# Optimization experiments

Hardware: AMD Instinct MI355X
Metric: run time of the kernel (lower is better)

## Reference

```python
import jax, jax.numpy as jnp
import numpy as np
from math import sqrt

B, TS_D, SEG, D, H = 16, 2, 1024, 256, 8
D_FF = 1024
DK = D // H
EPS = 1e-5


def _layernorm(x, g, b):
    mu = jnp.mean(x, axis=-1, keepdims=True)
    var = jnp.mean(jnp.square(x - mu), axis=-1, keepdims=True)
    return (x - mu) * jax.lax.rsqrt(var + EPS) * g + b


def setup_inputs() -> dict:
    key = jax.random.key(0)
    ks = jax.random.split(key, 16)
    s = 0.02
    return {
        "x": jax.random.normal(ks[0], (B, TS_D, SEG, D), dtype=jnp.float32),
        "Wq": jax.random.normal(ks[1], (D, D), dtype=jnp.float32) * s,
        "bq": jnp.zeros((D,), jnp.float32),
        "Wk": jax.random.normal(ks[2], (D, D), dtype=jnp.float32) * s,
        "bk": jnp.zeros((D,), jnp.float32),
        "Wv": jax.random.normal(ks[3], (D, D), dtype=jnp.float32) * s,
        "bv": jnp.zeros((D,), jnp.float32),
        "Wo": jax.random.normal(ks[4], (D, D), dtype=jnp.float32) * s,
        "bo": jnp.zeros((D,), jnp.float32),
        "g31": jnp.ones((D,), jnp.float32),
        "b31": jnp.zeros((D,), jnp.float32),
        "W1": jax.random.normal(ks[5], (D, D_FF), dtype=jnp.float32) * s,
        "b1": jnp.zeros((D_FF,), jnp.float32),
        "W2": jax.random.normal(ks[6], (D_FF, D), dtype=jnp.float32) * s,
        "b2": jnp.zeros((D,), jnp.float32),
        "g41": jnp.ones((D,), jnp.float32),
        "b41": jnp.zeros((D,), jnp.float32),
    }


def reference(x, Wq, bq, Wk, bk, Wv, bv, Wo, bo, g31, b31, W1, b1, W2, b2, g41, b41):
    # x: [B, ts_d=2, seg, d]; output is final_out2 (only live path of the module)
    b, ts_d, seg, d = x.shape
    scale = 1.0 / sqrt(DK)
    segments = x.reshape(b, ts_d * seg, d)            # [B, 2*seg, d]
    Q = (segments @ Wq + bq).reshape(b, -1, H, DK)
    K = (segments @ Wk + bk).reshape(b, -1, H, DK)
    V = (segments @ Wv + bv).reshape(b, -1, H, DK)
    q = Q[:, :seg]       # first seg positions (channel 0)
    k = K[:, -seg:]      # last seg positions (channel 1)
    v = V[:, -seg:]
    # cross-segment dual attention
    A1 = jax.nn.softmax(scale * jnp.einsum('blhe,bshe->bhls', q, k), axis=-1)
    out1 = jnp.einsum('bhls,bshd->blhd', A1, v).reshape(b, seg, d)
    A2 = jax.nn.softmax(scale * jnp.einsum('blhe,bshe->bhls', k, q), axis=-1)
    out2 = jnp.einsum('bhls,bshd->blhd', A2, q).reshape(b, seg, d)
    y = jnp.concatenate([out1, out2], axis=1) @ Wo + bo   # [B, 2*seg, d]
    h = _layernorm(segments + y, g31, b31)
    mlp = jax.nn.gelu(h @ W1 + b1, approximate=False) @ W2 + b2
    h = _layernorm(h + mlp, g41, b41)
    return h.reshape(b, ts_d, seg, d)
```

## Files before the change

### kernel.cpp

```cpp
#include <hip/hip_runtime.h>
#include <hip/hip_bf16.h>
#include <math.h>

#define BATCH 16
#define SEG 1024
#define DMODEL 256
#define NH 8
#define DK 32
#define DFF 1024
#define NTOK (BATCH * 2 * SEG)
#define EPS 1e-5f

typedef __attribute__((ext_vector_type(8))) short short8;
typedef __attribute__((ext_vector_type(4))) short short4b;
typedef __attribute__((ext_vector_type(4))) float f32x4;

#if __has_builtin(__builtin_amdgcn_exp2f)
#define EXP2(x) __builtin_amdgcn_exp2f(x)
#else
#define EXP2(x) __expf((x) * 0.6931471805599453f)
#endif

__device__ __forceinline__ ushort f2bf(float x) {
    union { float f; unsigned u; } a; a.f = x;
    unsigned r = a.u + 0x7fffu + ((a.u >> 16) & 1u);
    return (ushort)(r >> 16);
}

typedef const __attribute__((address_space(1))) unsigned gas_u32;
typedef __attribute__((address_space(3))) unsigned las_u32;
__device__ __forceinline__ void gload_lds16(const ushort* g, ushort* l) {
    __builtin_amdgcn_global_load_lds((gas_u32*)g, (las_u32*)l, 16, 0, 0);
}

__global__ __launch_bounds__(256) void wfrag_all_kernel(
    const float* __restrict__ Wq, const float* __restrict__ Wk,
    const float* __restrict__ Wv, const float* __restrict__ Wo,
    const float* __restrict__ W1, const float* __restrict__ W2,
    ushort* __restrict__ Wqf, ushort* __restrict__ Wkf,
    ushort* __restrict__ Wvf, ushort* __restrict__ Wof,
    ushort* __restrict__ W1f, ushort* __restrict__ W2f)
{
    const int blk = blockIdx.x;
    const float* src; ushort* dst; int K, N, order, base;
    if (blk < 32)       { src = Wq; dst = Wqf; K = 256;  N = 256;  order = 0; base = 0;   }
    else if (blk < 64)  { src = Wk; dst = Wkf; K = 256;  N = 256;  order = 0; base = 32;  }
    else if (blk < 96)  { src = Wv; dst = Wvf; K = 256;  N = 256;  order = 0; base = 64;  }
    else if (blk < 128) { src = Wo; dst = Wof; K = 256;  N = 256;  order = 0; base = 96;  }
    else if (blk < 256) { src = W1; dst = W1f; K = 256;  N = 1024; order = 0; base = 128; }
    else                { src = W2; dst = W2f; K = 1024; N = 256;  order = 1; base = 256; }
    const int tid = (blk - base) * 256 + threadIdx.x;
    const int KT_ = K >> 5, NT_ = N >> 4;
    const int lane = tid & 63;
    const int frag = tid >> 6;
    int kt, nt;
    if (order) { kt = frag / NT_; nt = frag % NT_; }
    else       { nt = frag / KT_; kt = frag % KT_; }
    const int quad = lane >> 4, l = lane & 15;
    const float* s = src + (size_t)(kt * 32 + quad * 8) * N + nt * 16 + l;
    short8 v;
#pragma unroll
    for (int j = 0; j < 8; j++) v[j] = (short)f2bf(s[(size_t)j * N]);
    *(short8*)&dst[(size_t)tid * 8] = v;
}

#define ASTR 264

__device__ __forceinline__ void dense256_pass(
    const ushort* __restrict__ Wf, ushort* WL, const short8* af,
    f32x4* acc, int t, int w, int lane)
{
#pragma unroll
    for (int nt = 0; nt < 16; ++nt) acc[nt] = (f32x4){0.f, 0.f, 0.f, 0.f};
    {
        const ushort* g = Wf + (size_t)w * 4096 + lane * 8;
        ushort* ld = WL + w * 4096;
#pragma unroll
        for (int i = 0; i < 8; ++i) gload_lds16(g + i * 512, ld + i * 512);
    }
    __syncthreads();
    for (int c = 0; c < 4; ++c) {
        if (c < 3) {
            const ushort* g = Wf + (size_t)(c + 1) * 16384 + w * 4096 + lane * 8;
            ushort* ld = WL + ((c + 1) & 1) * 8192 + w * 4096;
#pragma unroll
            for (int i = 0; i < 8; ++i) gload_lds16(g + i * 512, ld + i * 512);
        }
        const ushort* buf = WL + (c & 1) * 8192;
#pragma unroll
        for (int n2 = 0; n2 < 4; ++n2)
#pragma unroll
            for (int kt = 0; kt < 8; ++kt) {
                const short8 bf_ = *(const short8*)&buf[(n2 * 8 + kt) * 512 + lane * 8];
                acc[c * 4 + n2] = __builtin_amdgcn_mfma_f32_16x16x32_bf16(af[kt], bf_, acc[c * 4 + n2], 0, 0, 0);
            }
        __syncthreads();
    }
}

__global__ __launch_bounds__(256) void qkv_mfma_kernel(
    const float* __restrict__ x,
    const ushort* __restrict__ Wqf, const float* __restrict__ bq,
    const ushort* __restrict__ Wkf, const float* __restrict__ bk,
    const ushort* __restrict__ Wvf, const float* __restrict__ bv,
    ushort* __restrict__ qbuf, ushort* __restrict__ kbuf,
    ushort* __restrict__ qt, ushort* __restrict__ vt)
{
    __shared__ __align__(16) ushort SM[64 * ASTR];
    const int bid = blockIdx.x;
    const int which = bid >> 8;
    const int sub = bid & 255;
    const int b = sub >> 4, ti = sub & 15;
    const int half = (which == 0) ? 0 : 1;
    const int t = threadIdx.x;
    const int w = t >> 6, lane = t & 63, l = lane & 15, quad = lane >> 4;

    const float* xrow = x + ((size_t)b * 2048 + (size_t)half * 1024 + ti * 64) * 256;
#pragma unroll
    for (int p = 0; p < 16; ++p) {
        int ch = t + 256 * p;
        int row = ch >> 6, c4 = ch & 63;
        float4 v = *(const float4*)&xrow[row * 256 + c4 * 4];
        uint2 pk;
        pk.x = (unsigned)f2bf(v.x) | ((unsigned)f2bf(v.y) << 16);
        pk.y = (unsigned)f2bf(v.z) | ((unsigned)f2bf(v.w) << 16);
        *(uint2*)&SM[row * ASTR + c4 * 4] = pk;
    }
    __syncthreads();

    short8 af[8];
#pragma unroll
    for (int kt = 0; kt < 8; ++kt)
        af[kt] = *(const short8*)&SM[(w * 16 + l) * ASTR + kt * 32 + quad * 8];
    __syncthreads();

    const ushort* Wf  = (which == 0) ? Wqf : (which == 1 ? Wkf : Wvf);
    const float* bias = (which == 0) ? bq  : (which == 1 ? bk  : bv);
    const float kscale = (which == 1) ? 0.25503472f : 1.0f;

    f32x4 acc[16];
    dense256_pass(Wf, SM, af, acc, t, w, lane);

    ushort bfv[16][4];
#pragma unroll
    for (int nt = 0; nt < 16; ++nt) {
        const float bb = bias[nt * 16 + l];
#pragma unroll
        for (int r = 0; r < 4; ++r) bfv[nt][r] = f2bf((acc[nt][r] + bb) * kscale);
    }

    if (which <= 1) {
        ushort* obuf = which ? kbuf : qbuf;
#pragma unroll
        for (int nt = 0; nt < 16; ++nt) {
            const int h = nt >> 1, e = (nt & 1) * 16 + l;
#pragma unroll
            for (int r = 0; r < 4; ++r) {
                int tok = ti * 64 + w * 16 + quad * 4 + r;
                obuf[(((size_t)b * 8 + h) * SEG + tok) * 32 + e] = bfv[nt][r];
            }
        }
    }
    if (which != 1) {
        ushort* tb = which ? vt : qt;
#pragma unroll
        for (int nt = 0; nt < 16; ++nt)
#pragma unroll
            for (int r = 0; r < 4; ++r)
                SM[(nt * 16 + l) * 66 + w * 16 + quad * 4 + r] = bfv[nt][r];
        __syncthreads();
        const int d = t, hh = t >> 5, e = t & 31;
        ushort* dr = tb + (((size_t)b * 8 + hh) * 32 + e) * 1024 + ti * 64;
#pragma unroll
        for (int j = 0; j < 8; ++j) {
            uint2 v;
            v.x = *(const unsigned*)&SM[d * 66 + j * 8];
            v.y = *(const unsigned*)&SM[d * 66 + j * 8 + 2];
            unsigned z0 = *(const unsigned*)&SM[d * 66 + j * 8 + 4];
            unsigned z1 = *(const unsigned*)&SM[d * 66 + j * 8 + 6];
            *(uint4*)&dr[j * 8] = make_uint4(v.x, v.y, z0, z1);
        }
    }
}

#define KTILE 128
#define KP 40
#define VP 132

__global__ __launch_bounds__(256) void attn_mfma_kernel(
    const ushort* __restrict__ qbuf, const ushort* __restrict__ kbuf,
    const ushort* __restrict__ qt, const ushort* __restrict__ vt,
    ushort* __restrict__ abuf)
{
    __shared__ __align__(16) ushort Kl[KTILE * KP];
    __shared__ __align__(16) ushort Vl[32 * VP];

    const int bid   = blockIdx.x;
    const int sbh   = bid & 255;
    const int qtile = bid >> 8;
    const int stage = sbh >> 7;
    const int b     = (sbh >> 3) & 15;
    const int h     = sbh & 7;

    const ushort* Qm = stage ? kbuf : qbuf;
    const ushort* Km = stage ? qbuf : kbuf;
    const ushort* Vt = stage ? qt : vt;
    const size_t bh = ((size_t)b * 8 + h) * SEG * 32;

    const int t    = threadIdx.x;
    const int w    = t >> 6;
    const int lane = t & 63;
    const int l    = lane & 15;
    const int quad = lane >> 4;

    const int qrow = qtile * 64 + w * 16 + l;
    const short8 qf = *(const short8*)&Qm[bh + (size_t)qrow * 32 + quad * 8];

    f32x4 o0 = {0.f, 0.f, 0.f, 0.f};
    f32x4 o1 = {0.f, 0.f, 0.f, 0.f};
    f32x4 o2 = {0.f, 0.f, 0.f, 0.f};
    const short4b ones = {(short)0x3F80, (short)0x3F80, (short)0x3F80, (short)0x3F80};

    const int ch0 = t, ch1 = t + 256;
    const int kr0 = ((ch0 >> 6) << 4) | (ch0 & 15), kp0 = (ch0 >> 4) & 3;
    const int kr1 = ((ch1 >> 6) << 4) | (ch1 & 15), kp1 = (ch1 >> 4) & 3;
    const int vd0 = ch0 >> 4, vc0 = ch0 & 15;
    const int vd1 = ch1 >> 4, vc1 = ch1 & 15;
    const ushort* Kgb = &Km[bh];
    const ushort* Vgb = &Vt[bh];

    short8 rk0 = *(const short8*)&Kgb[(size_t)kr0 * 32 + kp0 * 8];
    short8 rk1 = *(const short8*)&Kgb[(size_t)kr1 * 32 + kp1 * 8];
    short8 rv0 = *(const short8*)&Vgb[(size_t)vd0 * 1024 + vc0 * 8];
    short8 rv1 = *(const short8*)&Vgb[(size_t)vd1 * 1024 + vc1 * 8];

    for (int tile = 0; tile < 8; ++tile) {
        __syncthreads();
        *(short8*)&Kl[kr0 * KP + kp0 * 8] = rk0;
        *(short8*)&Kl[kr1 * KP + kp1 * 8] = rk1;
        *(short8*)&Vl[vd0 * VP + vc0 * 8] = rv0;
        *(short8*)&Vl[vd1 * VP + vc1 * 8] = rv1;
        __syncthreads();

        if (tile < 7) {
            const size_t ko = (size_t)(tile + 1) * KTILE * 32;
            const size_t vo = (size_t)(tile + 1) * KTILE;
            rk0 = *(const short8*)&Kgb[ko + (size_t)kr0 * 32 + kp0 * 8];
            rk1 = *(const short8*)&Kgb[ko + (size_t)kr1 * 32 + kp1 * 8];
            rv0 = *(const short8*)&Vgb[vo + (size_t)vd0 * 1024 + vc0 * 8];
            rv1 = *(const short8*)&Vgb[vo + (size_t)vd1 * 1024 + vc1 * 8];
        }

#pragma unroll
        for (int kb = 0; kb < 8; ++kb) {
            const short8 kf = *(const short8*)&Kl[(kb * 16 + l) * KP + quad * 8];
            f32x4 z = {0.f, 0.f, 0.f, 0.f};
            f32x4 sc = __builtin_amdgcn_mfma_f32_16x16x32_bf16(kf, qf, z, 0, 0, 0);
            union { float f; unsigned u; } a0, a1, a2, a3;
            a0.f = EXP2(sc[0]); a1.f = EXP2(sc[1]);
            a2.f = EXP2(sc[2]); a3.f = EXP2(sc[3]);
            unsigned lo = __builtin_amdgcn_perm(a1.u, a0.u, 0x07060302u);
            unsigned hi = __builtin_amdgcn_perm(a3.u, a2.u, 0x07060302u);
            union { uint2 u; short4b s; } pk; pk.u = make_uint2(lo, hi);
            const short4b vf0 = *(const short4b*)&Vl[l * VP + kb * 16 + quad * 4];
            const short4b vf1 = *(const short4b*)&Vl[(16 + l) * VP + kb * 16 + quad * 4];
            o0 = __builtin_amdgcn_mfma_f32_16x16x16bf16_1k(vf0, pk.s, o0, 0, 0, 0);
            o1 = __builtin_amdgcn_mfma_f32_16x16x16bf16_1k(vf1, pk.s, o1, 0, 0, 0);
            o2 = __builtin_amdgcn_mfma_f32_16x16x16bf16_1k(ones, pk.s, o2, 0, 0, 0);
        }
    }

    const float inv = 1.0f / o2[0];
#pragma unroll
    for (int r = 0; r < 4; ++r) { o0[r] *= inv; o1[r] *= inv; }

    __syncthreads();
    ushort* Ob = &Kl[w * 16 * 40];
#pragma unroll
    for (int r = 0; r < 4; ++r) {
        Ob[l * 40 + quad * 4 + r]      = f2bf(o0[r]);
        Ob[l * 40 + 16 + quad * 4 + r] = f2bf(o1[r]);
    }
    __syncthreads();
    const int q = lane >> 2, part = lane & 3;
    const short8 ov = *(const short8*)&Ob[q * 40 + part * 8];
    const int tok = qtile * 64 + w * 16 + q;
    *(short8*)&abuf[((size_t)b * 2 * SEG + (size_t)stage * SEG + tok) * 256 + h * 32 + part * 8] = ov;
}

#define GP 40

__global__ __launch_bounds__(256, 2) void proj_mlp_kernel(
    const ushort* __restrict__ abuf, const ushort* __restrict__ Wof,
    const float* __restrict__ bo, const float* __restrict__ x,
    const float* __restrict__ g31, const float* __restrict__ b31,
    const ushort* __restrict__ W1f, const float* __restrict__ b1,
    const ushort* __restrict__ W2f, const float* __restrict__ b2,
    const float* __restrict__ g41, const float* __restrict__ b41,
    float* __restrict__ io)
{
    __shared__ __align__(16) ushort SM[2 * 16384];
    __shared__ __align__(16) ushort G[4][16 * GP];
    __shared__ __align__(16) float B1L[DFF];
    const int bid = blockIdx.x;
    const size_t tok0 = (size_t)bid * 64;
    const int t = threadIdx.x;
    const int w = t >> 6, lane = t & 63, l = lane & 15, quad = lane >> 4;

#pragma unroll
    for (int p = 0; p < 8; ++p) {
        int ch = t + 256 * p;
        int row = ch >> 5, c8 = ch & 31;
        *(short8*)&SM[row * ASTR + c8 * 8] = *(const short8*)&abuf[(tok0 + row) * 256 + c8 * 8];
    }
    *(float4*)&B1L[t * 4] = *(const float4*)&b1[t * 4];
    __syncthreads();

    short8 af[8];
#pragma unroll
    for (int kt = 0; kt < 8; ++kt)
        af[kt] = *(const short8*)&SM[(w * 16 + l) * ASTR + kt * 32 + quad * 8];
    __syncthreads();

    f32x4 acc[16];
    dense256_pass(Wof, SM, af, acc, t, w, lane);

#pragma unroll
    for (int nt = 0; nt < 16; ++nt) {
        const int d = nt * 16 + l;
        const float bv = bo[d];
#pragma unroll
        for (int r = 0; r < 4; ++r) {
            size_t tok = tok0 + w * 16 + quad * 4 + r;
            acc[nt][r] += bv + x[tok * 256 + d];
        }
    }
    {
        float mu_[4], is_[4];
#pragma unroll
        for (int r = 0; r < 4; ++r) {
            float s = 0.f;
#pragma unroll
            for (int nt = 0; nt < 16; ++nt) s += acc[nt][r];
            s += __shfl_xor(s, 1); s += __shfl_xor(s, 2);
            s += __shfl_xor(s, 4); s += __shfl_xor(s, 8);
            float mu = s * (1.0f / 256.0f);
            float vs = 0.f;
#pragma unroll
            for (int nt = 0; nt < 16; ++nt) { float dd = acc[nt][r] - mu; vs += dd * dd; }
            vs += __shfl_xor(vs, 1); vs += __shfl_xor(vs, 2);
            vs += __shfl_xor(vs, 4); vs += __shfl_xor(vs, 8);
            mu_[r] = mu;
            is_[r] = rsqrtf(vs * (1.0f / 256.0f) + EPS);
        }
#pragma unroll
        for (int nt = 0; nt < 16; ++nt) {
            const int d = nt * 16 + l;
            const float gg = g31[d], bb = b31[d];
#pragma unroll
            for (int r = 0; r < 4; ++r) {
                float hv = (acc[nt][r] - mu_[r]) * is_[r] * gg + bb;
                acc[nt][r] = hv;
                SM[(w * 16 + quad * 4 + r) * ASTR + d] = f2bf(hv);
            }
        }
    }
    __syncthreads();
#pragma unroll
    for (int kt = 0; kt < 8; ++kt)
        af[kt] = *(const short8*)&SM[(w * 16 + l) * ASTR + kt * 32 + quad * 8];
    __syncthreads();

    f32x4 out[16];
#pragma unroll
    for (int nt = 0; nt < 16; ++nt) out[nt] = (f32x4){0.f, 0.f, 0.f, 0.f};

    ushort* Gw = &G[w][0];

    {
        const ushort* g1 = W1f + w * 2048 + lane * 8;
        const ushort* g2 = W2f + w * 2048 + lane * 8;
        ushort* l1 = SM + w * 2048;
        ushort* l2 = SM + 8192 + w * 2048;
#pragma unroll
        for (int i = 0; i < 4; ++i) {
            gload_lds16(g1 + i * 512, l1 + i * 512);
            gload_lds16(g2 + i * 512, l2 + i * 512);
        }
    }
    __syncthreads();

    for (int c = 0; c < 32; ++c) {
        if (c < 31) {
            const int nb = (c + 1) & 1;
            const ushort* g1 = W1f + (size_t)(c + 1) * 8192 + w * 2048 + lane * 8;
            ushort* l1 = SM + nb * 16384 + w * 2048;
            const ushort* g2 = W2f + (size_t)(c + 1) * 8192 + w * 2048 + lane * 8;
            ushort* l2 = SM + nb * 16384 + 8192 + w * 2048;
#pragma unroll
            for (int i = 0; i < 4; ++i) {
                gload_lds16(g1 + i * 512, l1 + i * 512);
                gload_lds16(g2 + i * 512, l2 + i * 512);
            }
        }
        const ushort* WL = SM + (c & 1) * 16384;

        f32x4 s0 = {0.f, 0.f, 0.f, 0.f};
        f32x4 s1 = {0.f, 0.f, 0.f, 0.f};
#pragma unroll
        for (int kt = 0; kt < 8; ++kt) {
            const short8 b0 = *(const short8*)&WL[kt * 512 + lane * 8];
            const short8 b1_ = *(const short8*)&WL[(8 + kt) * 512 + lane * 8];
            s0 = __builtin_amdgcn_mfma_f32_16x16x32_bf16(af[kt], b0, s0, 0, 0, 0);
            s1 = __builtin_amdgcn_mfma_f32_16x16x32_bf16(af[kt], b1_, s1, 0, 0, 0);
        }

#pragma unroll
        for (int n2 = 0; n2 < 2; ++n2) {
            const float bv = B1L[c * 32 + n2 * 16 + l];
#pragma unroll
            for (int r = 0; r < 4; ++r) {
                float v = (n2 ? s1[r] : s0[r]) + bv;
                float au = fabsf(v) * 0.70710678118654752f;
                float t1 = __builtin_amdgcn_rcpf(fmaf(0.3275911f, au, 1.0f));
                float e  = EXP2(au * au * -1.4426950408889634f);
                float p5 = fmaf(fmaf(fmaf(fmaf(1.061405429f, t1, -1.453152027f),
                                t1, 1.421413741f), t1, -0.284496736f), t1, 0.254829592f) * t1;
                float erf_abs = fmaf(-p5, e, 1.0f);
                float gl = fmaf(0.5f * fabsf(v), erf_abs, 0.5f * v);
                Gw[(quad * 4 + r) * GP + n2 * 16 + l] = f2bf(gl);
            }
        }

        const short8 gf = *(const short8*)&Gw[l * GP + quad * 8];
#pragma unroll
        for (int nt = 0; nt < 16; ++nt) {
            const short8 bf_ = *(const short8*)&WL[8192 + nt * 512 + lane * 8];
            out[nt] = __builtin_amdgcn_mfma_f32_16x16x32_bf16(gf, bf_, out[nt], 0, 0, 0);
        }
        __syncthreads();
    }

#pragma unroll
    for (int nt = 0; nt < 16; ++nt) {
        const int d = nt * 16 + l;
        const float bv = b2[d];
#pragma unroll
        for (int r = 0; r < 4; ++r)
            out[nt][r] += bv + acc[nt][r];
    }

    float mu_[4], is_[4];
#pragma unroll
    for (int r = 0; r < 4; ++r) {
        float s = 0.f;
#pragma unroll
        for (int nt = 0; nt < 16; ++nt) s += out[nt][r];
        s += __shfl_xor(s, 1); s += __shfl_xor(s, 2);
        s += __shfl_xor(s, 4); s += __shfl_xor(s, 8);
        float mu = s * (1.0f / 256.0f);
        float vs = 0.f;
#pragma unroll
        for (int nt = 0; nt < 16; ++nt) { float dd = out[nt][r] - mu; vs += dd * dd; }
        vs += __shfl_xor(vs, 1); vs += __shfl_xor(vs, 2);
        vs += __shfl_xor(vs, 4); vs += __shfl_xor(vs, 8);
        mu_[r] = mu;
        is_[r] = rsqrtf(vs * (1.0f / 256.0f) + EPS);
    }

#pragma unroll
    for (int nt = 0; nt < 16; ++nt) {
        const int d = nt * 16 + l;
        const float gg = g41[d], bb = b41[d];
#pragma unroll
        for (int r = 0; r < 4; ++r) {
            size_t tok = tok0 + w * 16 + quad * 4 + r;
            io[tok * 256 + d] = (out[nt][r] - mu_[r]) * is_[r] * gg + bb;
        }
    }
}

extern "C" void kernel_launch(void* const* d_in, const int* in_sizes, int n_in,
                              void* d_out, int out_size, void* d_ws, size_t ws_size,
                              hipStream_t stream)
{
    const float* x   = (const float*)d_in[0];
    const float* Wq  = (const float*)d_in[1];
    const float* bq  = (const float*)d_in[2];
    const float* Wk  = (const float*)d_in[3];
    const float* bk  = (const float*)d_in[4];
    const float* Wv  = (const float*)d_in[5];
    const float* bv  = (const float*)d_in[6];
    const float* Wo  = (const float*)d_in[7];
    const float* bo  = (const float*)d_in[8];
    const float* g31 = (const float*)d_in[9];
    const float* b31 = (const float*)d_in[10];
    const float* W1  = (const float*)d_in[11];
    const float* b1  = (const float*)d_in[12];
    const float* W2  = (const float*)d_in[13];
    const float* b2  = (const float*)d_in[14];
    const float* g41 = (const float*)d_in[15];
    const float* b41 = (const float*)d_in[16];

    float* out = (float*)d_out;

    const size_t HALF = (size_t)BATCH * SEG * DMODEL;
    ushort* qbuf = (ushort*)d_ws;
    ushort* kbuf = qbuf + HALF;
    ushort* qt   = kbuf + HALF;
    ushort* vt   = qt + HALF;
    ushort* abuf = vt + HALF;
    ushort* Wqf  = abuf + 2 * HALF;
    ushort* Wkf  = Wqf + 65536;
    ushort* Wvf  = Wkf + 65536;
    ushort* Wof  = Wvf + 65536;
    ushort* W1f  = Wof + 65536;
    ushort* W2f  = W1f + 262144;

    wfrag_all_kernel<<<384, 256, 0, stream>>>(Wq, Wk, Wv, Wo, W1, W2,
                                              Wqf, Wkf, Wvf, Wof, W1f, W2f);

    qkv_mfma_kernel<<<768, 256, 0, stream>>>(x, Wqf, bq, Wkf, bk, Wvf, bv,
                                             qbuf, kbuf, qt, vt);
    attn_mfma_kernel<<<2 * BATCH * NH * (SEG / 64), 256, 0, stream>>>(qbuf, kbuf, qt, vt, abuf);
    proj_mlp_kernel<<<NTOK / 64, 256, 0, stream>>>(abuf, Wof, bo, x, g31, b31,
                                                   W1f, b1, W2f, b2, g41, b41, out);
}
```

Measured before the change: 266.1 us.

## Double block tokens to 128 with 512 threads and triple-buffer MLP weight pipeline

Each proj_mlp block now handles 128 tokens with 8 waves, so every weight tile staged into LDS is reused by twice as many rows and global weight traffic is halved. The Wo projection is rewritten as an inline double-buffered LDS-staged loop. The W1/W2 chunk loop moves from double to triple buffering, with explicit vmcnt waits and raw barriers so loads run two chunks ahead. LDS use grows to about 96KB+ per block, which may cut occupancy, and the hand-coded waitcnt logic is fragile.

```diff
diff --git a/kernel.cpp b/kernel.cpp
--- a/kernel.cpp
+++ b/kernel.cpp
@@ -290,7 +290,7 @@
 
 #define GP 40
 
-__global__ __launch_bounds__(256, 2) void proj_mlp_kernel(
+__global__ __launch_bounds__(512, 2) void proj_mlp_kernel(
     const ushort* __restrict__ abuf, const ushort* __restrict__ Wof,
     const float* __restrict__ bo, const float* __restrict__ x,
     const float* __restrict__ g31, const float* __restrict__ b31,
@@ -299,21 +299,21 @@
     const float* __restrict__ g41, const float* __restrict__ b41,
     float* __restrict__ io)
 {
-    __shared__ __align__(16) ushort SM[2 * 16384];
-    __shared__ __align__(16) ushort G[4][16 * GP];
+    __shared__ __align__(16) ushort SM[3 * 16384];
+    __shared__ __align__(16) ushort G[8][16 * GP];
     __shared__ __align__(16) float B1L[DFF];
     const int bid = blockIdx.x;
-    const size_t tok0 = (size_t)bid * 64;
+    const size_t tok0 = (size_t)bid * 128;
     const int t = threadIdx.x;
     const int w = t >> 6, lane = t & 63, l = lane & 15, quad = lane >> 4;
 
 #pragma unroll
     for (int p = 0; p < 8; ++p) {
-        int ch = t + 256 * p;
+        int ch = t + 512 * p;
         int row = ch >> 5, c8 = ch & 31;
         *(short8*)&SM[row * ASTR + c8 * 8] = *(const short8*)&abuf[(tok0 + row) * 256 + c8 * 8];
     }
-    *(float4*)&B1L[t * 4] = *(const float4*)&b1[t * 4];
+    *(float2*)&B1L[t * 2] = *(const float2*)&b1[t * 2];
     __syncthreads();
 
     short8 af[8];
@@ -323,7 +323,32 @@
     __syncthreads();
 
     f32x4 acc[16];
-    dense256_pass(Wof, SM, af, acc, t, w, lane);
+#pragma unroll
+    for (int nt = 0; nt < 16; ++nt) acc[nt] = (f32x4){0.f, 0.f, 0.f, 0.f};
+    {
+        const ushort* g = Wof + (size_t)w * 2048 + lane * 8;
+        ushort* ld = SM + w * 2048;
+#pragma unroll
+        for (int i = 0; i < 4; ++i) gload_lds16(g + i * 512, ld + i * 512);
+    }
+    __syncthreads();
+    for (int c = 0; c < 4; ++c) {
+        if (c < 3) {
+            const ushort* g = Wof + (size_t)(c + 1) * 16384 + w * 2048 + lane * 8;
+            ushort* ld = SM + ((c + 1) & 1) * 16384 + w * 2048;
+#pragma unroll
+            for (int i = 0; i < 4; ++i) gload_lds16(g + i * 512, ld + i * 512);
+        }
+        const ushort* buf = SM + (c & 1) * 16384;
+#pragma unroll
+        for (int n2 = 0; n2 < 4; ++n2)
+#pragma unroll
+            for (int kt = 0; kt < 8; ++kt) {
+                const short8 bf_ = *(const short8*)&buf[(n2 * 8 + kt) * 512 + lane * 8];
+                acc[c * 4 + n2] = __builtin_amdgcn_mfma_f32_16x16x32_bf16(af[kt], bf_, acc[c * 4 + n2], 0, 0, 0);
+            }
+        __syncthreads();
+    }
 
 #pragma unroll
     for (int nt = 0; nt < 16; ++nt) {
@@ -377,33 +402,36 @@
 
     ushort* Gw = &G[w][0];
 
+    const int wo = w * 1024 + lane * 8;
+    const int wl = w * 1024;
+
     {
-        const ushort* g1 = W1f + w * 2048 + lane * 8;
-        const ushort* g2 = W2f + w * 2048 + lane * 8;
-        ushort* l1 = SM + w * 2048;
-        ushort* l2 = SM + 8192 + w * 2048;
-#pragma unroll
-        for (int i = 0; i < 4; ++i) {
-            gload_lds16(g1 + i * 512, l1 + i * 512);
-            gload_lds16(g2 + i * 512, l2 + i * 512);
-        }
-    }
-    __syncthreads();
+        const ushort* g1 = W1f + wo;            ushort* l1 = SM + wl;
+        const ushort* g2 = W2f + wo;            ushort* l2 = SM + 8192 + wl;
+        gload_lds16(g1, l1); gload_lds16(g1 + 512, l1 + 512);
+        gload_lds16(g2, l2); gload_lds16(g2 + 512, l2 + 512);
+    }
+    {
+        const ushort* g1 = W1f + 8192 + wo;     ushort* l1 = SM + 16384 + wl;
+        const ushort* g2 = W2f + 8192 + wo;     ushort* l2 = SM + 16384 + 8192 + wl;
+        gload_lds16(g1, l1); gload_lds16(g1 + 512, l1 + 512);
+        gload_lds16(g2, l2); gload_lds16(g2 + 512, l2 + 512);
+    }
+    asm volatile("s_waitcnt vmcnt(4)" ::: "memory");
+    __builtin_amdgcn_s_barrier();
+    __builtin_amdgcn_sched_barrier(0);
 
     for (int c = 0; c < 32; ++c) {
-        if (c < 31) {
-            const int nb = (c + 1) & 1;
-            const ushort* g1 = W1f + (size_t)(c + 1) * 8192 + w * 2048 + lane * 8;
-            ushort* l1 = SM + nb * 16384 + w * 2048;
-            const ushort* g2 = W2f + (size_t)(c + 1) * 8192 + w * 2048 + lane * 8;
-            ushort* l2 = SM + nb * 16384 + 8192 + w * 2048;
-#pragma unroll
-            for (int i = 0; i < 4; ++i) {
-                gload_lds16(g1 + i * 512, l1 + i * 512);
-                gload_lds16(g2 + i * 512, l2 + i * 512);
-            }
-        }
-        const ushort* WL = SM + (c & 1) * 16384;
+        if (c < 30) {
+            const int s = (c + 2) % 3;
+            const ushort* g1 = W1f + (size_t)(c + 2) * 8192 + wo;
+            ushort* l1 = SM + s * 16384 + wl;
+            const ushort* g2 = W2f + (size_t)(c + 2) * 8192 + wo;
+            ushort* l2 = SM + s * 16384 + 8192 + wl;
+            gload_lds16(g1, l1); gload_lds16(g1 + 512, l1 + 512);
+            gload_lds16(g2, l2); gload_lds16(g2 + 512, l2 + 512);
+        }
+        const ushort* WL = SM + (c % 3) * 16384;
 
         f32x4 s0 = {0.f, 0.f, 0.f, 0.f};
         f32x4 s1 = {0.f, 0.f, 0.f, 0.f};
@@ -438,7 +466,11 @@
             const short8 bf_ = *(const short8*)&WL[8192 + nt * 512 + lane * 8];
             out[nt] = __builtin_amdgcn_mfma_f32_16x16x32_bf16(gf, bf_, out[nt], 0, 0, 0);
         }
-        __syncthreads();
+
+        if (c < 30) { asm volatile("s_waitcnt vmcnt(4)" ::: "memory"); }
+        else        { asm volatile("s_waitcnt vmcnt(0)" ::: "memory"); }
+        __builtin_amdgcn_s_barrier();
+        __builtin_amdgcn_sched_barrier(0);
     }
 
 #pragma unroll
@@ -523,6 +555,6 @@
     qkv_mfma_kernel<<<768, 256, 0, stream>>>(x, Wqf, bq, Wkf, bk, Wvf, bv,
                                              qbuf, kbuf, qt, vt);
     attn_mfma_kernel<<<2 * BATCH * NH * (SEG / 64), 256, 0, stream>>>(qbuf, kbuf, qt, vt, abuf);
-    proj_mlp_kernel<<<NTOK / 64, 256, 0, stream>>>(abuf, Wof, bo, x, g31, b31,
-                                                   W1f, b1, W2f, b2, g41, b41, out);
-}
+    proj_mlp_kernel<<<NTOK / 128, 512, 0, stream>>>(abuf, Wof, bo, x, g31, b31,
+                                                    W1f, b1, W2f, b2, g41, b41, out);
+}
```

New measurement: 268.9 us. No clear change (+1.1%).
